# Kernel tuning notes

Measured on AMD Instinct MI355X. Metric: run time of the kernel, lower is better.

## Reference

```python
import jax, jax.numpy as jnp
from jax import lax
import numpy as np

NUM_TOKENS = 2048
HIDDEN = 768
MAX_SPAN_WIDTH = 20
NUM_CAND = NUM_TOKENS * MAX_SPAN_WIDTH  # 40960
FEAT = 20
UNARY = 1024
SPAN_DIM = 3 * HIDDEN + FEAT  # 2324
MAX_NUM_SPANS = 512
TOP_SPAN_RATIO = 0.4


def setup_inputs() -> dict:
    key = jax.random.key(0)
    ks = jax.random.split(key, 16)
    starts = jax.random.randint(ks[0], (NUM_CAND,), 0, NUM_TOKENS, dtype=jnp.int32)
    widths = jax.random.randint(ks[1], (NUM_CAND,), 0, MAX_SPAN_WIDTH, dtype=jnp.int32)
    ends = jnp.minimum(starts + widths, NUM_TOKENS - 1)
    p = lambda k, shp: (0.02 * jax.random.normal(k, shp, dtype=jnp.float32))
    return {
        "hidden_states": jax.random.normal(ks[2], (NUM_TOKENS, HIDDEN), dtype=jnp.float32),
        "candidate_starts": starts,
        "candidate_ends": ends,
        "speaker_ids": jax.random.randint(ks[3], (NUM_TOKENS,), 0, 2, dtype=jnp.int32),
        "w_attn": p(ks[4], (HIDDEN,)),
        "b_attn": p(ks[5], ()),
        "W1": p(ks[6], (SPAN_DIM, UNARY)),
        "b1": p(ks[7], (UNARY,)),
        "W2": p(ks[8], (UNARY,)),
        "b2": p(ks[9], ()),
        "emb_width": p(ks[10], (MAX_SPAN_WIDTH, FEAT)),
        "emb_width_prior": p(ks[11], (MAX_SPAN_WIDTH, FEAT)),
        "Wp1": p(ks[12], (FEAT, UNARY)),
        "bp1": p(ks[13], (UNARY,)),
        "Wp2": p(ks[14], (UNARY,)),
        "bp2": p(ks[15], ()),
    }


def extract_spans(starts, ends, scores, num_top, num_words):
    """Greedy NMS-style span pruning: take spans by descending score, rejecting
    spans that partially overlap (cross) an already-accepted span; return
    num_top accepted candidate indices sorted by (start, end)."""
    order = jnp.argsort(-scores)  # descending score
    s_sorted = starts[order]
    e_sorted = ends[order]
    tok = jnp.arange(num_words, dtype=jnp.int32)

    def step(carry, se):
        latest_end, earliest_start, count = carry
        s, e = se
        in_range = (tok >= s) & (tok <= e)
        cross = jnp.any(in_range & (tok > s) & (latest_end > e)) | \
                jnp.any(in_range & (tok < e) & (earliest_start < s))
        accept = jnp.logical_and(~cross, count < num_top)
        latest_end = jnp.where(accept, latest_end.at[s].max(e), latest_end)
        earliest_start = jnp.where(accept, earliest_start.at[e].min(s), earliest_start)
        count = count + accept.astype(jnp.int32)
        return (latest_end, earliest_start, count), accept

    init = (jnp.full((num_words,), -1, jnp.int32),
            jnp.full((num_words,), num_words, jnp.int32),
            jnp.int32(0))
    (_, _, count), accepted = lax.scan(step, init, (s_sorted, e_sorted))
    # sort accepted spans by (start, end); push rejected to the back
    BIG = jnp.int32(np.iinfo(np.int32).max)
    sort_key = jnp.where(accepted, s_sorted * (num_words + 1) + e_sorted, BIG)
    by_pos = jnp.argsort(sort_key)
    picked = order[by_pos[:num_top]]
    # pad (if fewer than num_top accepted) with the first accepted span
    valid = jnp.arange(num_top) < count
    return jnp.where(valid, picked, picked[0])


def reference(hidden_states, candidate_starts, candidate_ends, speaker_ids,
              w_attn, b_attn, W1, b1, W2, b2,
              emb_width, emb_width_prior, Wp1, bp1, Wp2, bp2):
    num_words = hidden_states.shape[0]
    num_top_spans = int(min(MAX_NUM_SPANS, num_words * TOP_SPAN_RATIO))

    # masked softmax attention pooling over each span's tokens
    tok_att = hidden_states @ w_attn + b_attn            # [T]
    doc = jnp.arange(num_words, dtype=jnp.int32)
    token_mask = (doc[None, :] >= candidate_starts[:, None]) & \
                 (doc[None, :] <= candidate_ends[:, None])  # [C, T]
    logits = jnp.where(token_mask, tok_att[None, :], -jnp.inf)
    token_attn = jax.nn.softmax(logits, axis=1)          # [C, T]
    attended = token_attn @ hidden_states                # [C, H]

    width_idx = candidate_ends - candidate_starts        # in [0, MAX_SPAN_WIDTH)
    span_emb = jnp.concatenate([
        hidden_states[candidate_starts],
        hidden_states[candidate_ends],
        emb_width[width_idx],
        attended,
    ], axis=1)                                           # [C, 3H+F]

    h = jax.nn.relu(span_emb @ W1 + b1)
    span_scores = h @ W2 + b2                            # [C]
    hp = jax.nn.relu(emb_width_prior[width_idx] @ Wp1 + bp1)
    span_scores = span_scores + (hp @ Wp2 + bp2)

    pruned_idx = extract_spans(candidate_starts, candidate_ends,
                               lax.stop_gradient(span_scores),
                               num_top_spans, num_words)
    pruned_starts = candidate_starts[pruned_idx]
    pruned_ends = candidate_ends[pruned_idx]
    pruned_emb = span_emb[pruned_idx]
    pruned_scores = span_scores[pruned_idx]
    pruned_speaker_ids = speaker_ids[pruned_starts]
    return (span_emb, pruned_idx, pruned_starts, pruned_ends,
            pruned_emb, pruned_scores, pruned_speaker_ids)
```

## Files before the change

### kernel.cpp

```cpp
#include <hip/hip_runtime.h>
#include <math.h>

#define NT 2048
#define HID 768
#define NC 40960
#define NFEAT 20
#define UN 1024
#define SDIM 2324
#define NTOP 512
#define WMAX 20

#define NCOLS 1793
#define CHUNK 64
#define NCHUNK 32
#define CS_STRIDE 1800

#define OFF_IDX   95191040
#define OFF_S     95191552
#define OFF_E     95192064
#define OFF_PEMB  95192576
#define OFF_SC    96382464
#define OFF_SP    96382976

__global__ void k_zero(int* __restrict__ p, int n) {
  int i = blockIdx.x * 256 + threadIdx.x;
  if (i < n) p[i] = 0;
}

__global__ void k_hist(const int* __restrict__ starts, int* __restrict__ hist) {
  int i = blockIdx.x * 256 + threadIdx.x;
  atomicAdd(&hist[starts[i]], 1);
}

__global__ __launch_bounds__(256) void k_prefix(const int* __restrict__ hist,
                                                int* __restrict__ cursor) {
  __shared__ int tsum[256];
  int tid = threadIdx.x;
  int v[8], pre[8];
  int s = 0;
  #pragma unroll
  for (int j = 0; j < 8; ++j) { v[j] = hist[tid * 8 + j]; pre[j] = s; s += v[j]; }
  tsum[tid] = s;
  __syncthreads();
  for (int off = 1; off < 256; off <<= 1) {
    int t = (tid >= off) ? tsum[tid - off] : 0;
    __syncthreads();
    tsum[tid] += t;
    __syncthreads();
  }
  int base = (tid > 0) ? tsum[tid - 1] : 0;
  #pragma unroll
  for (int j = 0; j < 8; ++j) cursor[tid * 8 + j] = base + pre[j];
}

__global__ void k_place(const int* __restrict__ starts, int* __restrict__ cursor,
                        int* __restrict__ ord) {
  int i = blockIdx.x * 256 + threadIdx.x;
  int pos = atomicAdd(&cursor[starts[i]], 1);
  ord[pos] = i;
}

__global__ __launch_bounds__(256) void k_tok_att(const float* __restrict__ hidden,
                                                 const float* __restrict__ w_attn,
                                                 const float* __restrict__ b_attn,
                                                 float* __restrict__ expA) {
  int wave = (blockIdx.x * blockDim.x + threadIdx.x) >> 6;
  int lane = threadIdx.x & 63;
  if (wave >= NT) return;
  const float* row = hidden + (size_t)wave * HID;
  float s = 0.f;
  for (int c = lane; c < HID; c += 64) s += row[c] * w_attn[c];
  #pragma unroll
  for (int off = 32; off; off >>= 1) s += __shfl_down(s, off);
  if (lane == 0) expA[wave] = expf(s + b_attn[0]);
}

__global__ __launch_bounds__(256) void k_pc(const float* __restrict__ emb_width,
                                            const float* __restrict__ W1,
                                            float* __restrict__ Pc) {
  int idx = blockIdx.x * 256 + threadIdx.x;
  int w = idx >> 10, j = idx & 1023;
  float s = 0.f;
  #pragma unroll
  for (int k = 0; k < NFEAT; ++k) s += emb_width[w * NFEAT + k] * W1[(size_t)(2 * HID + k) * UN + j];
  Pc[idx] = s;
}

__global__ __launch_bounds__(256) void k_prior(const float* __restrict__ ewp,
                                               const float* __restrict__ Wp1,
                                               const float* __restrict__ bp1,
                                               const float* __restrict__ Wp2,
                                               const float* __restrict__ bp2,
                                               float* __restrict__ prior) {
  int w = blockIdx.x;
  int tid = threadIdx.x;
  __shared__ float red[256];
  float local = 0.f;
  for (int j = tid; j < UN; j += 256) {
    float hp = bp1[j];
    #pragma unroll
    for (int k = 0; k < NFEAT; ++k) hp += ewp[w * NFEAT + k] * Wp1[k * UN + j];
    local += fmaxf(hp, 0.f) * Wp2[j];
  }
  red[tid] = local;
  __syncthreads();
  for (int st = 128; st > 0; st >>= 1) { if (tid < st) red[tid] += red[tid + st]; __syncthreads(); }
  if (tid == 0) prior[w] = red[0] + bp2[0];
}

__global__ __launch_bounds__(256) void k_matmul_P(const float* __restrict__ hidden,
                                                  const float* __restrict__ W1,
                                                  float* __restrict__ P) {
  __shared__ float As[16][132];
  __shared__ float Bs[16][128];
  int bn = blockIdx.x, bm = blockIdx.y;
  int n0 = bn * 128;
  int seg = n0 >> 10;
  int rowbase = (seg == 0) ? 0 : (seg == 1 ? HID : (2 * HID + NFEAT));
  int j0 = n0 & 1023;
  int tid = threadIdx.x;
  int tx = tid & 15, ty = tid >> 4;
  float acc[8][8] = {};
  for (int k0 = 0; k0 < HID; k0 += 16) {
    #pragma unroll
    for (int q = 0; q < 2; ++q) {
      int idx = q * 256 + tid;
      int m = idx >> 2, kg = idx & 3;
      float4 a = *(const float4*)&hidden[(size_t)(bm * 128 + m) * HID + k0 + kg * 4];
      As[kg * 4 + 0][m] = a.x; As[kg * 4 + 1][m] = a.y;
      As[kg * 4 + 2][m] = a.z; As[kg * 4 + 3][m] = a.w;
      int k = idx >> 5, ng = idx & 31;
      float4 b = *(const float4*)&W1[(size_t)(rowbase + k0 + k) * UN + j0 + ng * 4];
      *(float4*)&Bs[k][ng * 4] = b;
    }
    __syncthreads();
    #pragma unroll
    for (int k = 0; k < 16; ++k) {
      float4 a0 = *(const float4*)&As[k][ty * 8];
      float4 a1 = *(const float4*)&As[k][ty * 8 + 4];
      float4 b0 = *(const float4*)&Bs[k][tx * 8];
      float4 b1 = *(const float4*)&Bs[k][tx * 8 + 4];
      float av[8] = {a0.x, a0.y, a0.z, a0.w, a1.x, a1.y, a1.z, a1.w};
      float bv[8] = {b0.x, b0.y, b0.z, b0.w, b1.x, b1.y, b1.z, b1.w};
      #pragma unroll
      for (int i = 0; i < 8; ++i)
        #pragma unroll
        for (int jj = 0; jj < 8; ++jj) acc[i][jj] += av[i] * bv[jj];
    }
    __syncthreads();
  }
  #pragma unroll
  for (int i = 0; i < 8; ++i) {
    float* prow = &P[(size_t)(bm * 128 + ty * 8 + i) * 3072 + n0 + tx * 8];
    *(float4*)prow = make_float4(acc[i][0], acc[i][1], acc[i][2], acc[i][3]);
    *(float4*)(prow + 4) = make_float4(acc[i][4], acc[i][5], acc[i][6], acc[i][7]);
  }
}

__global__ __launch_bounds__(256) void k_psumA(const float* __restrict__ hidden,
                                               const float* __restrict__ P,
                                               const float* __restrict__ expA,
                                               double* __restrict__ chunkSum) {
  int col = blockIdx.x * 256 + threadIdx.x;
  int ch = blockIdx.y;
  if (col >= NCOLS) return;
  double acc = 0.0;
  int t0 = ch * CHUNK;
  if (col < HID) {
    const float* p = hidden + col;
    #pragma unroll 8
    for (int r = 0; r < CHUNK; ++r) {
      int t = t0 + r;
      acc += (double)expA[t] * (double)p[(size_t)t * HID];
    }
  } else if (col < HID + UN) {
    const float* p = P + 2048 + (col - HID);
    #pragma unroll 8
    for (int r = 0; r < CHUNK; ++r) {
      int t = t0 + r;
      acc += (double)expA[t] * (double)p[(size_t)t * 3072];
    }
  } else {
    #pragma unroll 8
    for (int r = 0; r < CHUNK; ++r) acc += (double)expA[t0 + r];
  }
  chunkSum[(size_t)ch * CS_STRIDE + col] = acc;
}

__global__ __launch_bounds__(256) void k_psumB(double* __restrict__ chunkSum,
                                               double* __restrict__ prefH,
                                               double* __restrict__ prefPd,
                                               double* __restrict__ prefZ) {
  int col = blockIdx.x * 256 + threadIdx.x;
  if (col >= NCOLS) return;
  double run = 0.0;
  for (int ch = 0; ch < NCHUNK; ++ch) {
    size_t o = (size_t)ch * CS_STRIDE + col;
    double v = chunkSum[o];
    chunkSum[o] = run;
    run += v;
  }
  if (col < HID) prefH[col] = 0.0;
  else if (col < HID + UN) prefPd[col - HID] = 0.0;
  else prefZ[0] = 0.0;
}

__global__ __launch_bounds__(256) void k_psumC(const float* __restrict__ hidden,
                                               const float* __restrict__ P,
                                               const float* __restrict__ expA,
                                               const double* __restrict__ chunkSum,
                                               double* __restrict__ prefH,
                                               double* __restrict__ prefPd,
                                               double* __restrict__ prefZ) {
  int col = blockIdx.x * 256 + threadIdx.x;
  int ch = blockIdx.y;
  if (col >= NCOLS) return;
  double acc = chunkSum[(size_t)ch * CS_STRIDE + col];
  int t0 = ch * CHUNK;
  if (col < HID) {
    const float* p = hidden + col;
    double* o = prefH + col;
    #pragma unroll 4
    for (int r = 0; r < CHUNK; ++r) {
      int t = t0 + r;
      acc += (double)expA[t] * (double)p[(size_t)t * HID];
      o[(size_t)(t + 1) * HID] = acc;
    }
  } else if (col < HID + UN) {
    int c = col - HID;
    const float* p = P + 2048 + c;
    double* o = prefPd + c;
    #pragma unroll 4
    for (int r = 0; r < CHUNK; ++r) {
      int t = t0 + r;
      acc += (double)expA[t] * (double)p[(size_t)t * 3072];
      o[(size_t)(t + 1) * UN] = acc;
    }
  } else {
    #pragma unroll 4
    for (int r = 0; r < CHUNK; ++r) {
      int t = t0 + r;
      acc += (double)expA[t];
      prefZ[t + 1] = acc;
    }
  }
}

__global__ __launch_bounds__(256) void k_span(
    const int* __restrict__ ord,
    const float* __restrict__ hidden, const int* __restrict__ starts, const int* __restrict__ ends,
    const float* __restrict__ emb_width,
    const double* __restrict__ prefH, const double* __restrict__ prefPd,
    const double* __restrict__ prefZ,
    const float* __restrict__ P, const float* __restrict__ Pc,
    const float* __restrict__ b1, const float* __restrict__ W2,
    const float* __restrict__ b2ptr, const float* __restrict__ prior,
    float* __restrict__ out, float* __restrict__ scores, unsigned long long* __restrict__ keys) {
  int i = ord[blockIdx.x];
  int s = starts[i], e = ends[i];
  int w = e - s;
  int tid = threadIdx.x;
  double invZ = 1.0 / (prefZ[e + 1] - prefZ[s]);
  const float* hs = hidden + (size_t)s * HID;
  const float* he = hidden + (size_t)e * HID;
  const double* pHs = prefH + (size_t)s * HID;
  const double* pHe = prefH + (size_t)(e + 1) * HID;
  float* orow = out + (size_t)i * SDIM;
  for (int q = tid; q < SDIM / 4; q += 256) {
    int c = q * 4;
    float4 v;
    if (c < HID) v = *(const float4*)(hs + c);
    else if (c < 2 * HID) v = *(const float4*)(he + (c - HID));
    else if (c < 2 * HID + NFEAT) v = *(const float4*)(emb_width + w * NFEAT + (c - 2 * HID));
    else {
      int cc = c - (2 * HID + NFEAT);
      const double* pe = pHe + cc;
      const double* ps = pHs + cc;
      v = make_float4((float)((pe[0] - ps[0]) * invZ),
                      (float)((pe[1] - ps[1]) * invZ),
                      (float)((pe[2] - ps[2]) * invZ),
                      (float)((pe[3] - ps[3]) * invZ));
    }
    *(float4*)(orow + c) = v;
  }
  int j = tid * 4;
  float4 pre = *(const float4*)(b1 + j);
  float4 pa = *(const float4*)(P + (size_t)s * 3072 + j);
  float4 pb = *(const float4*)(P + (size_t)e * 3072 + 1024 + j);
  float4 pc = *(const float4*)(Pc + w * UN + j);
  const double* pds = prefPd + (size_t)s * UN + j;
  const double* pde = prefPd + (size_t)(e + 1) * UN + j;
  pre.x += pa.x + pb.x + pc.x + (float)((pde[0] - pds[0]) * invZ);
  pre.y += pa.y + pb.y + pc.y + (float)((pde[1] - pds[1]) * invZ);
  pre.z += pa.z + pb.z + pc.z + (float)((pde[2] - pds[2]) * invZ);
  pre.w += pa.w + pb.w + pc.w + (float)((pde[3] - pds[3]) * invZ);
  float4 w2 = *(const float4*)(W2 + j);
  float local = fmaxf(pre.x, 0.f) * w2.x + fmaxf(pre.y, 0.f) * w2.y +
                fmaxf(pre.z, 0.f) * w2.z + fmaxf(pre.w, 0.f) * w2.w;
  #pragma unroll
  for (int off = 32; off; off >>= 1) local += __shfl_down(local, off);
  __shared__ float red[4];
  if ((tid & 63) == 0) red[tid >> 6] = local;
  __syncthreads();
  if (tid == 0) {
    float sc = red[0] + red[1] + red[2] + red[3] + b2ptr[0] + prior[w];
    scores[i] = sc;
    unsigned u = __float_as_uint(sc);
    u = (u >> 31) ? ~u : (u | 0x80000000u);
    unsigned inv = ~u;
    keys[i] = (((unsigned long long)inv) << 32) | (unsigned)i;
  }
}

__global__ __launch_bounds__(256) void k_rank(const unsigned long long* __restrict__ keys,
                                              int* __restrict__ rank) {
  int ic = blockIdx.x >> 5;
  int jc = blockIdx.x & 31;
  int tid = threadIdx.x;
  int ibase = ic * 2048 + tid;
  unsigned long long mk[8];
  int cnt[8];
  #pragma unroll
  for (int k = 0; k < 8; ++k) { mk[k] = keys[ibase + k * 256]; cnt[k] = 0; }
  int j0 = jc * 1280;
  #pragma unroll 4
  for (int j = j0; j < j0 + 1280; ++j) {
    unsigned long long kj = keys[j];
    #pragma unroll
    for (int k = 0; k < 8; ++k) cnt[k] += (kj < mk[k]) ? 1 : 0;
  }
  #pragma unroll
  for (int k = 0; k < 8; ++k) if (cnt[k]) atomicAdd(&rank[ibase + k * 256], cnt[k]);
}

__global__ void k_scatter(const int* __restrict__ rank, int* __restrict__ order) {
  int i = blockIdx.x * 256 + threadIdx.x;
  order[rank[i]] = i;
}

__global__ void k_scan(const int* __restrict__ order,
                       const int* __restrict__ starts,
                       const int* __restrict__ ends,
                       int* __restrict__ acc_idx, int* __restrict__ acc_s,
                       int* __restrict__ acc_e, int* __restrict__ acc_count) {
  __shared__ int LE[NT];
  __shared__ int ES[NT];
  int lane = threadIdx.x;
  for (int t = lane; t < NT; t += 64) { LE[t] = -1; ES[t] = NT; }
  __syncthreads();
  int count = 0;
  for (int base = 0; base < NC && count < NTOP; base += 64) {
    int ci = order[base + lane];
    int sv = starts[ci];
    int ev = ends[ci];
    bool pc = false;
    for (int t = sv; t <= ev; ++t) {
      int l = LE[t], es2 = ES[t];
      pc = pc || ((t > sv) && (l > ev)) || ((t < ev) && (es2 < sv));
    }
    unsigned long long pm = __ballot(pc);
    int localCount = 0;
    int ls = 0, le = -1, li = 0;
    for (int t = 0; t < 64; ++t) {
      int s = __shfl(sv, t);
      int e = __shfl(ev, t);
      int cidx = __shfl(ci, t);
      bool ov = (lane < localCount) &&
                (((s < ls) && (ls <= e) && (e < le)) ||
                 ((ls < s) && (s <= le) && (le < e)));
      bool cross = (((pm >> t) & 1ull) != 0) || __any(ov);
      if (!cross) {
        if (lane == localCount) { ls = s; le = e; li = cidx; }
        localCount++;
        count++;
        if (count >= NTOP) break;
      }
    }
    int cbase = count - localCount;
    if (lane < localCount) {
      acc_idx[cbase + lane] = li;
      acc_s[cbase + lane] = ls;
      acc_e[cbase + lane] = le;
      atomicMax(&LE[ls], le);
      atomicMin(&ES[le], ls);
    }
    __syncthreads();
  }
  if (lane == 0) acc_count[0] = count;
}

__global__ __launch_bounds__(512) void k_outputs(const int* __restrict__ acc_idx,
                                                 const int* __restrict__ acc_s,
                                                 const int* __restrict__ acc_e,
                                                 const int* __restrict__ acc_count,
                                                 const float* __restrict__ scores,
                                                 const int* __restrict__ speaker,
                                                 float* __restrict__ out,
                                                 int* __restrict__ sortedIdx) {
  __shared__ int ks[NTOP];
  int tid = threadIdx.x;
  int count = acc_count[0];
  int key = 0x7FFFFFFF;
  if (tid < count) key = acc_s[tid] * (NT + 1) + acc_e[tid];
  ks[tid] = key;
  __syncthreads();
  if (tid < count) {
    int r = 0;
    for (int b = 0; b < count; ++b) {
      int kb = ks[b];
      r += ((kb < key) || (kb == key && b < tid)) ? 1 : 0;
    }
    int ci = acc_idx[tid];
    out[OFF_IDX + r] = (float)ci;
    out[OFF_S + r]   = (float)acc_s[tid];
    out[OFF_E + r]   = (float)acc_e[tid];
    out[OFF_SC + r]  = scores[ci];
    out[OFF_SP + r]  = (float)speaker[acc_s[tid]];
    sortedIdx[r] = ci;
  }
  __syncthreads();
  if (tid >= count) {
    out[OFF_IDX + tid] = out[OFF_IDX];
    out[OFF_S + tid]   = out[OFF_S];
    out[OFF_E + tid]   = out[OFF_E];
    out[OFF_SC + tid]  = out[OFF_SC];
    out[OFF_SP + tid]  = out[OFF_SP];
    sortedIdx[tid] = sortedIdx[0];
  }
}

__global__ __launch_bounds__(256) void k_copy_emb(const int* __restrict__ sortedIdx,
                                                  float* __restrict__ out) {
  int r = blockIdx.x;
  int ci = sortedIdx[r];
  const float* src = out + (size_t)ci * SDIM;
  float* dst = out + OFF_PEMB + (size_t)r * SDIM;
  for (int q = threadIdx.x; q < SDIM / 4; q += 256) {
    ((float4*)dst)[q] = ((const float4*)src)[q];
  }
}

extern "C" void kernel_launch(void* const* d_in, const int* in_sizes, int n_in,
                              void* d_out, int out_size, void* d_ws, size_t ws_size,
                              hipStream_t stream) {
  const float* hidden   = (const float*)d_in[0];
  const int*   starts   = (const int*)d_in[1];
  const int*   ends     = (const int*)d_in[2];
  const int*   speaker  = (const int*)d_in[3];
  const float* w_attn   = (const float*)d_in[4];
  const float* b_attn   = (const float*)d_in[5];
  const float* W1       = (const float*)d_in[6];
  const float* b1       = (const float*)d_in[7];
  const float* W2       = (const float*)d_in[8];
  const float* b2       = (const float*)d_in[9];
  const float* embw     = (const float*)d_in[10];
  const float* ewp      = (const float*)d_in[11];
  const float* Wp1      = (const float*)d_in[12];
  const float* bp1      = (const float*)d_in[13];
  const float* Wp2      = (const float*)d_in[14];
  const float* bp2      = (const float*)d_in[15];
  float* out = (float*)d_out;

  float* f = (float*)d_ws;
  float* P       = f;
  float* expA    = P + 6291456;
  float* Pc      = expA + 2048;
  float* prior   = Pc + 20480;
  float* scores  = prior + 32;
  unsigned long long* keys = (unsigned long long*)(scores + 40960);
  double* prefPd = (double*)(keys + 40960);
  double* prefZ  = prefPd + 2049 * 1024;
  double* chunkSum = prefZ + 2056;
  double* prefH  = chunkSum + 32 * CS_STRIDE;
  int* rank      = (int*)(prefH + 2049 * 768);
  int* order     = rank + 40960;
  int* acc_idx   = order + 40960;
  int* acc_s     = acc_idx + NTOP;
  int* acc_e     = acc_s + NTOP;
  int* acc_count = acc_e + NTOP;
  int* sortedIdx = acc_count + 4;
  int* hist      = sortedIdx + NTOP;
  int* cursor    = hist + NT;
  int* ord       = cursor + NT;

  k_zero<<<dim3(8), dim3(256), 0, stream>>>(hist, NT);
  k_zero<<<dim3(160), dim3(256), 0, stream>>>(rank, NC);
  k_hist<<<dim3(160), dim3(256), 0, stream>>>(starts, hist);
  k_prefix<<<dim3(1), dim3(256), 0, stream>>>(hist, cursor);
  k_place<<<dim3(160), dim3(256), 0, stream>>>(starts, cursor, ord);

  k_tok_att<<<dim3(512), dim3(256), 0, stream>>>(hidden, w_attn, b_attn, expA);
  k_pc<<<dim3(80), dim3(256), 0, stream>>>(embw, W1, Pc);
  k_prior<<<dim3(20), dim3(256), 0, stream>>>(ewp, Wp1, bp1, Wp2, bp2, prior);
  k_matmul_P<<<dim3(24, 16), dim3(256), 0, stream>>>(hidden, W1, P);

  k_psumA<<<dim3(8, NCHUNK), dim3(256), 0, stream>>>(hidden, P, expA, chunkSum);
  k_psumB<<<dim3(8), dim3(256), 0, stream>>>(chunkSum, prefH, prefPd, prefZ);
  k_psumC<<<dim3(8, NCHUNK), dim3(256), 0, stream>>>(hidden, P, expA, chunkSum,
                                                     prefH, prefPd, prefZ);

  k_span<<<dim3(NC), dim3(256), 0, stream>>>(ord, hidden, starts, ends, embw,
                                             prefH, prefPd, prefZ, P, Pc,
                                             b1, W2, b2, prior, out, scores, keys);
  k_rank<<<dim3(640), dim3(256), 0, stream>>>(keys, rank);
  k_scatter<<<dim3(160), dim3(256), 0, stream>>>(rank, order);
  k_scan<<<dim3(1), dim3(64), 0, stream>>>(order, starts, ends, acc_idx, acc_s, acc_e, acc_count);
  k_outputs<<<dim3(1), dim3(512), 0, stream>>>(acc_idx, acc_s, acc_e, acc_count, scores,
                                               speaker, out, sortedIdx);
  k_copy_emb<<<dim3(NTOP), dim3(256), 0, stream>>>(sortedIdx, out);
}
```

Measured before the change: 1.042 ms.

## Prefilter top-scoring candidates by radix bucket before ranking and NMS scan

Builds a 16-bit histogram of score keys, finds a cutoff bucket that keeps at least the top 8192 candidates, and compacts those survivors. It ranks and scans only the survivors instead of doing an all-pairs rank over all 40960 candidates. A flagged fallback path reruns the full rank, scatter and scan when the survivors yield fewer than 512 accepted spans. The scan loop also iterates only over lanes that are not pre-rejected, using ffs, and stops once the top-512 count is reached. This adds several small launches and extra workspace in exchange for cutting the quadratic ranking work.

```diff
diff --git a/kernel.cpp b/kernel.cpp
--- a/kernel.cpp
+++ b/kernel.cpp
@@ -9,6 +9,7 @@
 #define SDIM 2324
 #define NTOP 512
 #define WMAX 20
+#define TOPT 8192
 
 #define NCOLS 1793
 #define CHUNK 64
@@ -312,8 +313,148 @@
   }
 }
 
-__global__ __launch_bounds__(256) void k_rank(const unsigned long long* __restrict__ keys,
-                                              int* __restrict__ rank) {
+__global__ void k_bucket(const unsigned long long* __restrict__ keys,
+                         int* __restrict__ hist64k) {
+  int i = blockIdx.x * 256 + threadIdx.x;
+  atomicAdd(&hist64k[(int)(keys[i] >> 48)], 1);
+}
+
+__global__ __launch_bounds__(1024) void k_cutoff(const int* __restrict__ hist64k,
+                                                 int* __restrict__ cutB) {
+  __shared__ int psum[1024];
+  int tid = threadIdx.x;
+  int base = tid * 64;
+  int s = 0;
+  #pragma unroll
+  for (int j = 0; j < 16; ++j) {
+    int4 v = *(const int4*)&hist64k[base + j * 4];
+    s += v.x + v.y + v.z + v.w;
+  }
+  psum[tid] = s;
+  __syncthreads();
+  for (int off = 1; off < 1024; off <<= 1) {
+    int t = (tid >= off) ? psum[tid - off] : 0;
+    __syncthreads();
+    psum[tid] += t;
+    __syncthreads();
+  }
+  int cumEnd = psum[tid];
+  int cumStart = cumEnd - s;
+  if (cumStart < TOPT && TOPT <= cumEnd) {
+    int run = cumStart;
+    for (int j = 0; j < 64; ++j) {
+      run += hist64k[base + j];
+      if (run >= TOPT) { cutB[0] = base + j; break; }
+    }
+  }
+}
+
+__global__ void k_compact(const unsigned long long* __restrict__ keys,
+                          const int* __restrict__ cutB,
+                          int* __restrict__ survCount,
+                          int* __restrict__ surv,
+                          unsigned long long* __restrict__ survKey) {
+  int i = blockIdx.x * 256 + threadIdx.x;
+  int B = cutB[0];
+  unsigned long long k = keys[i];
+  bool keep = ((int)(k >> 48)) <= B;
+  unsigned long long m = __ballot(keep);
+  if (m == 0ull) return;
+  int lane = threadIdx.x & 63;
+  int leader = __ffsll((long long)m) - 1;
+  int pos = 0;
+  if (lane == leader) pos = atomicAdd(survCount, __popcll(m));
+  pos = __shfl(pos, leader);
+  if (keep) {
+    int slot = pos + __popcll(m & ((1ull << lane) - 1ull));
+    surv[slot] = i;
+    survKey[slot] = k;
+  }
+}
+
+__global__ __launch_bounds__(256) void k_rankT(const unsigned long long* __restrict__ survKey,
+                                               const int* __restrict__ survCount,
+                                               int* __restrict__ rankS) {
+  int S = survCount[0];
+  int i = blockIdx.x * 256 + threadIdx.x;
+  int j0 = blockIdx.y * 1280;
+  if (i >= S || j0 >= S) return;
+  int j1 = min(j0 + 1280, S);
+  unsigned long long mk = survKey[i];
+  int cnt = 0;
+  for (int j = j0; j < j1; ++j) cnt += (survKey[j] < mk) ? 1 : 0;
+  if (cnt) atomicAdd(&rankS[i], cnt);
+}
+
+__global__ void k_scatterT(const int* __restrict__ surv, const int* __restrict__ rankS,
+                           const int* __restrict__ survCount, int* __restrict__ order) {
+  int t = blockIdx.x * 256 + threadIdx.x;
+  if (t < survCount[0]) order[rankS[t]] = surv[t];
+}
+
+__global__ void k_scanT(const int* __restrict__ order,
+                        const int* __restrict__ starts,
+                        const int* __restrict__ ends,
+                        const int* __restrict__ survCount,
+                        int* __restrict__ acc_idx, int* __restrict__ acc_s,
+                        int* __restrict__ acc_e, int* __restrict__ acc_count,
+                        int* __restrict__ flag) {
+  __shared__ int LE[NT];
+  __shared__ int ES[NT];
+  int lane = threadIdx.x;
+  int S = survCount[0];
+  for (int t = lane; t < NT; t += 64) { LE[t] = -1; ES[t] = NT; }
+  __syncthreads();
+  int count = 0;
+  for (int base = 0; base < S && count < NTOP; base += 64) {
+    int idx = base + lane;
+    bool valid = idx < S;
+    int ci = order[valid ? idx : 0];
+    int sv = starts[ci];
+    int ev = ends[ci];
+    bool pc = !valid;
+    for (int t = sv; t <= ev; ++t) {
+      int l = LE[t], es2 = ES[t];
+      pc = pc || ((t > sv) && (l > ev)) || ((t < ev) && (es2 < sv));
+    }
+    unsigned long long rem = ~__ballot(pc);
+    int localCount = 0;
+    int ls = 0, le = -1, li = 0;
+    while (rem != 0ull && count < NTOP) {
+      int t = __ffsll((long long)rem) - 1;
+      rem &= rem - 1;
+      int s = __shfl(sv, t);
+      int e = __shfl(ev, t);
+      int cidx = __shfl(ci, t);
+      bool ov = (lane < localCount) &&
+                (((s < ls) && (ls <= e) && (e < le)) ||
+                 ((ls < s) && (s <= le) && (le < e)));
+      if (!__any(ov)) {
+        if (lane == localCount) { ls = s; le = e; li = cidx; }
+        localCount++;
+        count++;
+      }
+    }
+    int cbase = count - localCount;
+    if (lane < localCount) {
+      acc_idx[cbase + lane] = li;
+      acc_s[cbase + lane] = ls;
+      acc_e[cbase + lane] = le;
+      atomicMax(&LE[ls], le);
+      atomicMin(&ES[le], ls);
+    }
+    __syncthreads();
+  }
+  if (lane == 0) {
+    acc_count[0] = count;
+    flag[0] = (count < NTOP && S < NC) ? 1 : 0;
+  }
+}
+
+__global__ __launch_bounds__(256) void k_rank_fb(const int* __restrict__ flag,
+                                                 const unsigned long long* __restrict__ keys,
+                                                 int* __restrict__ rank2) {
+  if (!flag[0]) return;
   int ic = blockIdx.x >> 5;
   int jc = blockIdx.x & 31;
   int tid = threadIdx.x;
@@ -330,19 +471,23 @@
     for (int k = 0; k < 8; ++k) cnt[k] += (kj < mk[k]) ? 1 : 0;
   }
   #pragma unroll
-  for (int k = 0; k < 8; ++k) if (cnt[k]) atomicAdd(&rank[ibase + k * 256], cnt[k]);
-}
-
-__global__ void k_scatter(const int* __restrict__ rank, int* __restrict__ order) {
+  for (int k = 0; k < 8; ++k) if (cnt[k]) atomicAdd(&rank2[ibase + k * 256], cnt[k]);
+}
+
+__global__ void k_scatter_fb(const int* __restrict__ flag, const int* __restrict__ rank2,
+                             int* __restrict__ orderFB) {
+  if (!flag[0]) return;
   int i = blockIdx.x * 256 + threadIdx.x;
-  order[rank[i]] = i;
-}
-
-__global__ void k_scan(const int* __restrict__ order,
-                       const int* __restrict__ starts,
-                       const int* __restrict__ ends,
-                       int* __restrict__ acc_idx, int* __restrict__ acc_s,
-                       int* __restrict__ acc_e, int* __restrict__ acc_count) {
+  orderFB[rank2[i]] = i;
+}
+
+__global__ void k_scan_fb(const int* __restrict__ flag,
+                          const int* __restrict__ orderFB,
+                          const int* __restrict__ starts,
+                          const int* __restrict__ ends,
+                          int* __restrict__ acc_idx, int* __restrict__ acc_s,
+                          int* __restrict__ acc_e, int* __restrict__ acc_count) {
+  if (!flag[0]) return;
   __shared__ int LE[NT];
   __shared__ int ES[NT];
   int lane = threadIdx.x;
@@ -350,7 +495,7 @@
   __syncthreads();
   int count = 0;
   for (int base = 0; base < NC && count < NTOP; base += 64) {
-    int ci = order[base + lane];
+    int ci = orderFB[base + lane];
     int sv = starts[ci];
     int ev = ends[ci];
     bool pc = false;
@@ -358,22 +503,22 @@
       int l = LE[t], es2 = ES[t];
       pc = pc || ((t > sv) && (l > ev)) || ((t < ev) && (es2 < sv));
     }
-    unsigned long long pm = __ballot(pc);
+    unsigned long long rem = ~__ballot(pc);
     int localCount = 0;
     int ls = 0, le = -1, li = 0;
-    for (int t = 0; t < 64; ++t) {
+    while (rem != 0ull && count < NTOP) {
+      int t = __ffsll((long long)rem) - 1;
+      rem &= rem - 1;
       int s = __shfl(sv, t);
       int e = __shfl(ev, t);
       int cidx = __shfl(ci, t);
       bool ov = (lane < localCount) &&
                 (((s < ls) && (ls <= e) && (e < le)) ||
                  ((ls < s) && (s <= le) && (le < e)));
-      bool cross = (((pm >> t) & 1ull) != 0) || __any(ov);
-      if (!cross) {
+      if (!__any(ov)) {
         if (lane == localCount) { ls = s; le = e; li = cidx; }
         localCount++;
         count++;
-        if (count >= NTOP) break;
       }
     }
     int cbase = count - localCount;
@@ -472,19 +617,29 @@
   double* prefZ  = prefPd + 2049 * 1024;
   double* chunkSum = prefZ + 2056;
   double* prefH  = chunkSum + 32 * CS_STRIDE;
-  int* rank      = (int*)(prefH + 2049 * 768);
-  int* order     = rank + 40960;
-  int* acc_idx   = order + 40960;
+  int* rankS     = (int*)(prefH + 2049 * 768);
+  int* rank2     = rankS + 40960;
+  int* order     = rank2 + 40960;
+  int* orderFB   = order + 40960;
+  int* acc_idx   = orderFB + 40960;
   int* acc_s     = acc_idx + NTOP;
   int* acc_e     = acc_s + NTOP;
   int* acc_count = acc_e + NTOP;
-  int* sortedIdx = acc_count + 4;
+  int* flag      = acc_count + 4;
+  int* sortedIdx = flag + 4;
   int* hist      = sortedIdx + NTOP;
   int* cursor    = hist + NT;
   int* ord       = cursor + NT;
+  int* hist64k   = ord + 40960;
+  int* survCount = hist64k + 65536;
+  int* cutB      = survCount + 4;
+  int* surv      = cutB + 4;
+  unsigned long long* survKey = (unsigned long long*)(surv + 40960);
 
   k_zero<<<dim3(8), dim3(256), 0, stream>>>(hist, NT);
-  k_zero<<<dim3(160), dim3(256), 0, stream>>>(rank, NC);
+  k_zero<<<dim3(320), dim3(256), 0, stream>>>(rankS, 2 * NC);
+  k_zero<<<dim3(257), dim3(256), 0, stream>>>(hist64k, 65536 + 8);
+
   k_hist<<<dim3(160), dim3(256), 0, stream>>>(starts, hist);
   k_prefix<<<dim3(1), dim3(256), 0, stream>>>(hist, cursor);
   k_place<<<dim3(160), dim3(256), 0, stream>>>(starts, cursor, ord);
@@ -502,9 +657,20 @@
   k_span<<<dim3(NC), dim3(256), 0, stream>>>(ord, hidden, starts, ends, embw,
                                              prefH, prefPd, prefZ, P, Pc,
                                              b1, W2, b2, prior, out, scores, keys);
-  k_rank<<<dim3(640), dim3(256), 0, stream>>>(keys, rank);
-  k_scatter<<<dim3(160), dim3(256), 0, stream>>>(rank, order);
-  k_scan<<<dim3(1), dim3(64), 0, stream>>>(order, starts, ends, acc_idx, acc_s, acc_e, acc_count);
+
+  k_bucket<<<dim3(160), dim3(256), 0, stream>>>(keys, hist64k);
+  k_cutoff<<<dim3(1), dim3(1024), 0, stream>>>(hist64k, cutB);
+  k_compact<<<dim3(160), dim3(256), 0, stream>>>(keys, cutB, survCount, surv, survKey);
+  k_rankT<<<dim3(160, 32), dim3(256), 0, stream>>>(survKey, survCount, rankS);
+  k_scatterT<<<dim3(160), dim3(256), 0, stream>>>(surv, rankS, survCount, order);
+  k_scanT<<<dim3(1), dim3(64), 0, stream>>>(order, starts, ends, survCount,
+                                            acc_idx, acc_s, acc_e, acc_count, flag);
+
+  k_rank_fb<<<dim3(640), dim3(256), 0, stream>>>(flag, keys, rank2);
+  k_scatter_fb<<<dim3(160), dim3(256), 0, stream>>>(flag, rank2, orderFB);
+  k_scan_fb<<<dim3(1), dim3(64), 0, stream>>>(flag, orderFB, starts, ends,
+                                              acc_idx, acc_s, acc_e, acc_count);
+
   k_outputs<<<dim3(1), dim3(512), 0, stream>>>(acc_idx, acc_s, acc_e, acc_count, scores,
                                                speaker, out, sortedIdx);
   k_copy_emb<<<dim3(NTOP), dim3(256), 0, stream>>>(sortedIdx, out);
```

After: 1.002 ms. 1.04x faster.
